# Kernel optimization log

Measured on AMD Instinct MI355X. Metric: run time of the kernel, lower is better.

## Reference

```python
import jax, jax.numpy as jnp
import numpy as np
from jax import lax

H, W, K, B = 64, 64, 64, 64
OFFSETS = [(0, 1), (2, 1), (1, 0), (1, 2)]  # up, down, left, right slices into padded grid


def setup_inputs() -> dict:
    key = jax.random.key(0)
    ks = jax.random.split(key, 7)
    n = H * W * 3
    s = lambda d: 1.0 / np.sqrt(d)
    return {
        "obs_flat": jax.random.normal(ks[0], (B, n), jnp.float32),
        "phi_w": jax.random.normal(ks[1], (n, n), jnp.float32) * s(n),
        "phi_b": jax.random.normal(ks[2], (n,), jnp.float32) * s(n),
        "w1": jax.random.normal(ks[3], (36, 16), jnp.float32) * s(36),
        "b1": jax.random.normal(ks[4], (16,), jnp.float32) * s(36),
        "w2": jax.random.normal(ks[5], (16, 4), jnp.float32) * s(16),
        "b2": jax.random.normal(ks[6], (4,), jnp.float32) * s(16),
    }


def _vin(rin, rout, p):
    # rin, rout, p: [B, H, W]. K Bellman-style 4-neighbor sweeps.
    prin = jnp.pad(rin, ((0, 0), (1, 1), (1, 1)))
    rin_sh = jnp.stack([prin[:, ho:ho + H, wo:wo + W] for ho, wo in OFFSETS])  # [4,B,H,W]
    rout_masked = rout[None] * (rin_sh != 0).astype(rin.dtype)                 # [4,B,H,W]

    def step(V, _):
        pv = jnp.pad(V, ((0, 0), (1, 1), (1, 1)))
        v_sh = jnp.stack([pv[:, ho:ho + H, wo:wo + W] for ho, wo in OFFSETS])
        nv = p[None] * v_sh + rin_sh - rout_masked
        return jnp.maximum(V, nv.max(axis=0)), None

    V0 = jnp.zeros_like(rin)
    V, _ = lax.scan(step, V0, None, length=K)
    return V


def reference(obs_flat, phi_w, phi_b, w1, b1, w2, b2):
    obs = obs_flat.reshape(B, H, W, 3)
    phi = (obs_flat @ phi_w + phi_b).reshape(B, H, W, 3)
    rin, rout = phi[..., 0], phi[..., 1]
    p = jax.nn.softmax(phi[..., 2].reshape(B, H * W), axis=1).reshape(B, H, W)

    V = _vin(rin, rout, p)  # [B,H,W]
    obs_val = jnp.concatenate([obs, V[..., None]], axis=-1)  # [B,H,W,4]
    padded = jnp.pad(obs_val, ((0, 0), (1, 1), (1, 1), (0, 0)))

    # agent position = location of the (one-hot) nonzero in channel 1
    flat = jnp.argmax(obs[..., 1].reshape(B, -1), axis=1)
    pi, pj = flat // W, flat % W
    patch = jax.vmap(lambda x, i, j: lax.dynamic_slice(x, (i, j, 0), (3, 3, 4)))(padded, pi, pj)

    h = jax.nn.relu(patch.reshape(B, 36) @ w1 + b1)
    logit = h @ w2 + b2  # [B, 4]
    return logit
```

## Files before the change

kernel.cpp:

```cpp
#include <hip/hip_runtime.h>
#include <hip/hip_bf16.h>

typedef __attribute__((ext_vector_type(8))) short short8;
typedef __attribute__((ext_vector_type(4))) float floatx4;
typedef __attribute__((ext_vector_type(4))) unsigned short ushort4v;
typedef __attribute__((ext_vector_type(8))) unsigned short ushort8v;

#define N_DIM 12288
#define SPLITK 4
#define KCHUNK (N_DIM / SPLITK)
#define KSTEP 64
#define NTILE 64

__device__ __forceinline__ unsigned short f2bf(float f) {
  union { float f; unsigned int i; } x; x.f = f;
  unsigned int r = x.i + 0x7fffu + ((x.i >> 16) & 1u);
  return (unsigned short)(r >> 16);
}

__global__ __launch_bounds__(256) void gemm_phi(
    const float* __restrict__ obs, const float* __restrict__ W,
    const float* __restrict__ bias, float* __restrict__ phi)
{
  __shared__ unsigned short A_s[64 * 72];
  __shared__ unsigned short W_s[64 * 72];

  const int t = threadIdx.x;
  const int n0 = blockIdx.x * NTILE;
  const int s  = blockIdx.y;
  const int k0 = s * KCHUNK;
  const int lane = t & 63, wv = t >> 6;
  const int l16 = lane & 15, q = lane >> 4;
  const int m0f = 16 * wv;

  floatx4 acc[4];
#pragma unroll
  for (int i = 0; i < 4; i++) acc[i] = (floatx4){0.f, 0.f, 0.f, 0.f};

  const int am = t >> 2, akq = (t & 3) * 16;
  const int rg = t >> 4, cg = t & 15;

  for (int it = 0; it < KCHUNK / KSTEP; ++it) {
    const int kb = k0 + it * KSTEP;
    {
      const float* src = obs + (size_t)am * N_DIM + kb + akq;
      floatx4 f0 = *(const floatx4*)(src);
      floatx4 f1 = *(const floatx4*)(src + 4);
      floatx4 f2 = *(const floatx4*)(src + 8);
      floatx4 f3 = *(const floatx4*)(src + 12);
      ushort8v u0, u1;
#pragma unroll
      for (int i = 0; i < 4; i++) {
        u0[i] = f2bf(f0[i]); u0[4 + i] = f2bf(f1[i]);
        u1[i] = f2bf(f2[i]); u1[4 + i] = f2bf(f3[i]);
      }
      *(ushort8v*)&A_s[am * 72 + akq]     = u0;
      *(ushort8v*)&A_s[am * 72 + akq + 8] = u1;
    }
    {
      const size_t base = (size_t)(kb + 4 * rg) * N_DIM + (n0 + 4 * cg);
      floatx4 r0 = *(const floatx4*)(W + base);
      floatx4 r1 = *(const floatx4*)(W + base + N_DIM);
      floatx4 r2 = *(const floatx4*)(W + base + 2 * N_DIM);
      floatx4 r3 = *(const floatx4*)(W + base + 3 * N_DIM);
#pragma unroll
      for (int i = 0; i < 4; i++) {
        ushort4v v = { f2bf(r0[i]), f2bf(r1[i]), f2bf(r2[i]), f2bf(r3[i]) };
        *(ushort4v*)&W_s[(4 * cg + i) * 72 + 4 * rg] = v;
      }
    }
    __syncthreads();
#pragma unroll
    for (int kk = 0; kk < 2; ++kk) {
      short8 af = *(const short8*)&A_s[(m0f + l16) * 72 + 32 * kk + 8 * q];
#pragma unroll
      for (int nt = 0; nt < 4; ++nt) {
        short8 wf = *(const short8*)&W_s[(16 * nt + l16) * 72 + 32 * kk + 8 * q];
        acc[nt] = __builtin_amdgcn_mfma_f32_16x16x32_bf16(af, wf, acc[nt], 0, 0, 0);
      }
    }
    __syncthreads();
  }
#pragma unroll
  for (int nt = 0; nt < 4; ++nt) {
    const int ncol = n0 + 16 * nt + l16;
    const float bv = (s == 0) ? bias[ncol] : 0.f;
#pragma unroll
    for (int r = 0; r < 4; ++r) {
      const int m = m0f + q * 4 + r;
      atomicAdd(&phi[(size_t)m * N_DIM + ncol], acc[nt][r] + bv);
    }
  }
}

#define VSTR 76
#define VOFF(h, w) (((h) + 1) * VSTR + (w) + 4)

__global__ __launch_bounds__(256) void vin_mlp(
    const float* __restrict__ obs, const float* __restrict__ phi,
    const float* __restrict__ w1, const float* __restrict__ b1,
    const float* __restrict__ w2, const float* __restrict__ b2,
    float* __restrict__ out)
{
  __shared__ float Vb[2][66 * VSTR];
  __shared__ float red_v[256];
  __shared__ int   red_i[256];

  const int b = blockIdx.x;
  const int t = threadIdx.x;
  const int ty = t >> 4, tx = t & 15;
  const int h0 = ty * 4, w0 = tx * 4;

  for (int i = t; i < 2 * 66 * VSTR; i += 256) (&Vb[0][0])[i] = 0.f;

  float rin[16], rout[16], lg[16];
#pragma unroll
  for (int r = 0; r < 4; r++) {
    const int j = 3 * ((h0 + r) * 64 + w0);
    const floatx4* p4 = (const floatx4*)(phi + (size_t)b * N_DIM + j);
    floatx4 x0 = p4[0], x1 = p4[1], x2 = p4[2];
    float f[12];
#pragma unroll
    for (int c = 0; c < 4; c++) { f[c] = x0[c]; f[4 + c] = x1[c]; f[8 + c] = x2[c]; }
#pragma unroll
    for (int c = 0; c < 4; c++) {
      rin [r * 4 + c] = f[3 * c + 0];
      rout[r * 4 + c] = f[3 * c + 1];
      lg  [r * 4 + c] = f[3 * c + 2];
    }
  }

  float lmax = -3.4e38f;
#pragma unroll
  for (int i = 0; i < 16; i++) lmax = fmaxf(lmax, lg[i]);
  __syncthreads();
  red_v[t] = lmax; __syncthreads();
  for (int o = 128; o > 0; o >>= 1) { if (t < o) red_v[t] = fmaxf(red_v[t], red_v[t + o]); __syncthreads(); }
  const float M = red_v[0];
  __syncthreads();
  float p[16]; float esum = 0.f;
#pragma unroll
  for (int i = 0; i < 16; i++) { p[i] = __expf(lg[i] - M); esum += p[i]; }
  red_v[t] = esum; __syncthreads();
  for (int o = 128; o > 0; o >>= 1) { if (t < o) red_v[t] += red_v[t + o]; __syncthreads(); }
  const float inv = 1.f / red_v[0];
  __syncthreads();
#pragma unroll
  for (int i = 0; i < 16; i++) p[i] *= inv;

#pragma unroll
  for (int r = 0; r < 4; r++) {
    floatx4 rr = { rin[r * 4 + 0], rin[r * 4 + 1], rin[r * 4 + 2], rin[r * 4 + 3] };
    *(floatx4*)&Vb[1][VOFF(h0 + r, w0)] = rr;
  }
  __syncthreads();
  float cu[16], cdn[16], cl[16], cr[16];
#pragma unroll
  for (int r = 0; r < 4; r++) {
#pragma unroll
    for (int c = 0; c < 4; c++) {
      const int i = r * 4 + c, h = h0 + r, w = w0 + c;
      const float nu = Vb[1][VOFF(h - 1, w)];
      const float nd = Vb[1][VOFF(h + 1, w)];
      const float nl = Vb[1][VOFF(h, w - 1)];
      const float nr = Vb[1][VOFF(h, w + 1)];
      cu [i] = nu - (nu != 0.f ? rout[i] : 0.f);
      cdn[i] = nd - (nd != 0.f ? rout[i] : 0.f);
      cl [i] = nl - (nl != 0.f ? rout[i] : 0.f);
      cr [i] = nr - (nr != 0.f ? rout[i] : 0.f);
    }
  }
  __syncthreads();

  float v[16];
#pragma unroll
  for (int i = 0; i < 16; i++) v[i] = 0.f;

  for (int k = 0; k < 64; k++) {
    const float* Vc = Vb[k & 1];
    float* Vn = Vb[(k & 1) ^ 1];
    const floatx4 top = *(const floatx4*)&Vc[VOFF(h0 - 1, w0)];
    const floatx4 bot = *(const floatx4*)&Vc[VOFF(h0 + 4, w0)];
    float lf[4], rt[4];
#pragma unroll
    for (int r = 0; r < 4; r++) { lf[r] = Vc[VOFF(h0 + r, w0 - 1)]; rt[r] = Vc[VOFF(h0 + r, w0 + 4)]; }
    float nv[16];
#pragma unroll
    for (int r = 0; r < 4; r++) {
#pragma unroll
      for (int c = 0; c < 4; c++) {
        const int i = r * 4 + c;
        const float vu = (r == 0) ? top[c] : v[i - 4];
        const float vd = (r == 3) ? bot[c] : v[i + 4];
        const float vl = (c == 0) ? lf[r] : v[i - 1];
        const float vr = (c == 3) ? rt[r] : v[i + 1];
        const float m1 = fmaxf(fmaf(p[i], vu, cu[i]), fmaf(p[i], vd, cdn[i]));
        const float m2 = fmaxf(fmaf(p[i], vl, cl[i]), fmaf(p[i], vr, cr[i]));
        nv[i] = fmaxf(v[i], fmaxf(m1, m2));
      }
    }
#pragma unroll
    for (int r = 0; r < 4; r++) {
      floatx4 w4 = { nv[r * 4 + 0], nv[r * 4 + 1], nv[r * 4 + 2], nv[r * 4 + 3] };
      *(floatx4*)&Vn[VOFF(h0 + r, w0)] = w4;
    }
#pragma unroll
    for (int i = 0; i < 16; i++) v[i] = nv[i];
    __syncthreads();
  }

  float amax = -3.4e38f; int aidx = 0;
#pragma unroll
  for (int r = 0; r < 4; r++) {
#pragma unroll
    for (int c = 0; c < 4; c++) {
      const int cell = (h0 + r) * 64 + (w0 + c);
      const float val = obs[(size_t)b * N_DIM + 3 * cell + 1];
      if (val > amax) { amax = val; aidx = cell; }
    }
  }
  red_v[t] = amax; red_i[t] = aidx;
  __syncthreads();
  for (int o = 128; o > 0; o >>= 1) {
    if (t < o) {
      const float v2 = red_v[t + o]; const int i2 = red_i[t + o];
      if (v2 > red_v[t] || (v2 == red_v[t] && i2 < red_i[t])) { red_v[t] = v2; red_i[t] = i2; }
    }
    __syncthreads();
  }
  const int pos = red_i[0];
  const int pi = pos >> 6, pj = pos & 63;
  __syncthreads();

  if (t < 36) {
    const int di = t / 12, rem = t % 12, dj = rem / 4, c4 = rem & 3;
    const int hh = pi - 1 + di, ww = pj - 1 + dj;
    float pv;
    if (c4 < 3) {
      pv = (hh >= 0 && hh < 64 && ww >= 0 && ww < 64)
           ? obs[(size_t)b * N_DIM + 3 * (hh * 64 + ww) + c4] : 0.f;
    } else {
      pv = Vb[0][VOFF(hh, ww)];
    }
    red_v[t] = pv;
  }
  __syncthreads();
  if (t < 16) {
    float a = b1[t];
#pragma unroll
    for (int j = 0; j < 36; j++) a = fmaf(red_v[j], w1[j * 16 + t], a);
    red_v[64 + t] = fmaxf(a, 0.f);
  }
  __syncthreads();
  if (t < 4) {
    float a = b2[t];
#pragma unroll
    for (int i = 0; i < 16; i++) a = fmaf(red_v[64 + i], w2[i * 4 + t], a);
    out[b * 4 + t] = a;
  }
}

extern "C" void kernel_launch(void* const* d_in, const int* in_sizes, int n_in,
                              void* d_out, int out_size, void* d_ws, size_t ws_size,
                              hipStream_t stream)
{
  (void)in_sizes; (void)n_in; (void)out_size; (void)ws_size;
  const float* obs  = (const float*)d_in[0];
  const float* phiw = (const float*)d_in[1];
  const float* phib = (const float*)d_in[2];
  const float* w1   = (const float*)d_in[3];
  const float* b1   = (const float*)d_in[4];
  const float* w2   = (const float*)d_in[5];
  const float* b2   = (const float*)d_in[6];
  float* phi = (float*)d_ws;
  float* out = (float*)d_out;

  hipMemsetAsync(phi, 0, (size_t)64 * N_DIM * sizeof(float), stream);
  hipLaunchKernelGGL(gemm_phi, dim3(N_DIM / NTILE, SPLITK), dim3(256), 0, stream,
                     obs, phiw, phib, phi);
  hipLaunchKernelGGL(vin_mlp, dim3(64), dim3(256), 0, stream,
                     obs, phi, w1, b1, w2, b2, out);
}
```

Before: 836.8 us.

## Double-buffer A tile, load W fragments directly to registers, raise split-K

Restructures the phi GEMM so each wave owns 16 output columns and loads its W fragment straight from global memory into registers, dropping the shared-memory transpose of W. The A tile is double-buffered in LDS and the next iteration's A and W loads are issued before the current MFMAs, leaving one barrier per step. Split-K rises from 4 to 8 to put more blocks on the device, in exchange for twice as many atomic adds into phi. The W loads are scalar strided reads, 16 lanes wide per row, which may hurt coalescing.

Result: no change. 841.9 us (+0.6%).

```diff
diff --git a/kernel.cpp b/kernel.cpp
--- a/kernel.cpp
+++ b/kernel.cpp
@@ -3,14 +3,12 @@
 
 typedef __attribute__((ext_vector_type(8))) short short8;
 typedef __attribute__((ext_vector_type(4))) float floatx4;
-typedef __attribute__((ext_vector_type(4))) unsigned short ushort4v;
 typedef __attribute__((ext_vector_type(8))) unsigned short ushort8v;
 
 #define N_DIM 12288
-#define SPLITK 4
+#define SPLITK 8
 #define KCHUNK (N_DIM / SPLITK)
-#define KSTEP 64
-#define NTILE 64
+#define NIT (KCHUNK / 64)
 
 __device__ __forceinline__ unsigned short f2bf(float f) {
   union { float f; unsigned int i; } x; x.f = f;
@@ -22,73 +20,100 @@
     const float* __restrict__ obs, const float* __restrict__ W,
     const float* __restrict__ bias, float* __restrict__ phi)
 {
-  __shared__ unsigned short A_s[64 * 72];
-  __shared__ unsigned short W_s[64 * 72];
+  __shared__ unsigned short A_s[2][64 * 72];
 
   const int t = threadIdx.x;
-  const int n0 = blockIdx.x * NTILE;
+  const int n0 = blockIdx.x * 64;
   const int s  = blockIdx.y;
   const int k0 = s * KCHUNK;
   const int lane = t & 63, wv = t >> 6;
   const int l16 = lane & 15, q = lane >> 4;
-  const int m0f = 16 * wv;
+  const int nc = n0 + 16 * wv + l16;
 
   floatx4 acc[4];
 #pragma unroll
   for (int i = 0; i < 4; i++) acc[i] = (floatx4){0.f, 0.f, 0.f, 0.f};
 
-  const int am = t >> 2, akq = (t & 3) * 16;
-  const int rg = t >> 4, cg = t & 15;
-
-  for (int it = 0; it < KCHUNK / KSTEP; ++it) {
-    const int kb = k0 + it * KSTEP;
-    {
-      const float* src = obs + (size_t)am * N_DIM + kb + akq;
-      floatx4 f0 = *(const floatx4*)(src);
-      floatx4 f1 = *(const floatx4*)(src + 4);
-      floatx4 f2 = *(const floatx4*)(src + 8);
-      floatx4 f3 = *(const floatx4*)(src + 12);
+  const int am = t >> 2, ak = (t & 3) * 16;
+  const float* Ap = obs + (size_t)am * N_DIM + k0 + ak;
+  const float* Bp = W + (size_t)(k0 + 8 * q) * N_DIM + nc;
+
+  float fb[16];
+  {
+    floatx4 fA[4];
+#pragma unroll
+    for (int i = 0; i < 4; i++) fA[i] = *(const floatx4*)(Ap + 4 * i);
+    ushort8v u0, u1;
+#pragma unroll
+    for (int i = 0; i < 4; i++) {
+      u0[i] = f2bf(fA[0][i]); u0[4 + i] = f2bf(fA[1][i]);
+      u1[i] = f2bf(fA[2][i]); u1[4 + i] = f2bf(fA[3][i]);
+    }
+    *(ushort8v*)&A_s[0][am * 72 + ak]     = u0;
+    *(ushort8v*)&A_s[0][am * 72 + ak + 8] = u1;
+#pragma unroll
+    for (int kk = 0; kk < 2; ++kk)
+#pragma unroll
+      for (int j = 0; j < 8; ++j)
+        fb[kk * 8 + j] = Bp[(size_t)(32 * kk + j) * N_DIM];
+  }
+  __syncthreads();
+
+#pragma unroll 2
+  for (int it = 0; it < NIT; ++it) {
+    const int cur = it & 1;
+    const bool more = (it + 1 < NIT);
+    floatx4 fA[4];
+    float fbn[16];
+    if (more) {
+      const float* ap = Ap + (it + 1) * 64;
+#pragma unroll
+      for (int i = 0; i < 4; i++) fA[i] = *(const floatx4*)(ap + 4 * i);
+      const float* bp = Bp + (size_t)(it + 1) * 64 * N_DIM;
+#pragma unroll
+      for (int kk = 0; kk < 2; ++kk)
+#pragma unroll
+        for (int j = 0; j < 8; ++j)
+          fbn[kk * 8 + j] = bp[(size_t)(32 * kk + j) * N_DIM];
+    }
+    short8 bfr0, bfr1;
+#pragma unroll
+    for (int j = 0; j < 8; ++j) {
+      bfr0[j] = (short)f2bf(fb[j]);
+      bfr1[j] = (short)f2bf(fb[8 + j]);
+    }
+#pragma unroll
+    for (int mt = 0; mt < 4; ++mt) {
+      short8 af0 = *(const short8*)&A_s[cur][(16 * mt + l16) * 72 + 8 * q];
+      acc[mt] = __builtin_amdgcn_mfma_f32_16x16x32_bf16(af0, bfr0, acc[mt], 0, 0, 0);
+    }
+#pragma unroll
+    for (int mt = 0; mt < 4; ++mt) {
+      short8 af1 = *(const short8*)&A_s[cur][(16 * mt + l16) * 72 + 32 + 8 * q];
+      acc[mt] = __builtin_amdgcn_mfma_f32_16x16x32_bf16(af1, bfr1, acc[mt], 0, 0, 0);
+    }
+    if (more) {
       ushort8v u0, u1;
 #pragma unroll
       for (int i = 0; i < 4; i++) {
-        u0[i] = f2bf(f0[i]); u0[4 + i] = f2bf(f1[i]);
-        u1[i] = f2bf(f2[i]); u1[4 + i] = f2bf(f3[i]);
+        u0[i] = f2bf(fA[0][i]); u0[4 + i] = f2bf(fA[1][i]);
+        u1[i] = f2bf(fA[2][i]); u1[4 + i] = f2bf(fA[3][i]);
       }
-      *(ushort8v*)&A_s[am * 72 + akq]     = u0;
-      *(ushort8v*)&A_s[am * 72 + akq + 8] = u1;
-    }
-    {
-      const size_t base = (size_t)(kb + 4 * rg) * N_DIM + (n0 + 4 * cg);
-      floatx4 r0 = *(const floatx4*)(W + base);
-      floatx4 r1 = *(const floatx4*)(W + base + N_DIM);
-      floatx4 r2 = *(const floatx4*)(W + base + 2 * N_DIM);
-      floatx4 r3 = *(const floatx4*)(W + base + 3 * N_DIM);
-#pragma unroll
-      for (int i = 0; i < 4; i++) {
-        ushort4v v = { f2bf(r0[i]), f2bf(r1[i]), f2bf(r2[i]), f2bf(r3[i]) };
-        *(ushort4v*)&W_s[(4 * cg + i) * 72 + 4 * rg] = v;
-      }
+      *(ushort8v*)&A_s[cur ^ 1][am * 72 + ak]     = u0;
+      *(ushort8v*)&A_s[cur ^ 1][am * 72 + ak + 8] = u1;
+#pragma unroll
+      for (int i = 0; i < 16; i++) fb[i] = fbn[i];
     }
     __syncthreads();
-#pragma unroll
-    for (int kk = 0; kk < 2; ++kk) {
-      short8 af = *(const short8*)&A_s[(m0f + l16) * 72 + 32 * kk + 8 * q];
-#pragma unroll
-      for (int nt = 0; nt < 4; ++nt) {
-        short8 wf = *(const short8*)&W_s[(16 * nt + l16) * 72 + 32 * kk + 8 * q];
-        acc[nt] = __builtin_amdgcn_mfma_f32_16x16x32_bf16(af, wf, acc[nt], 0, 0, 0);
-      }
-    }
-    __syncthreads();
-  }
-#pragma unroll
-  for (int nt = 0; nt < 4; ++nt) {
-    const int ncol = n0 + 16 * nt + l16;
-    const float bv = (s == 0) ? bias[ncol] : 0.f;
+  }
+
+  const float bv = (s == 0) ? bias[nc] : 0.f;
+#pragma unroll
+  for (int mt = 0; mt < 4; ++mt) {
 #pragma unroll
     for (int r = 0; r < 4; ++r) {
-      const int m = m0f + q * 4 + r;
-      atomicAdd(&phi[(size_t)m * N_DIM + ncol], acc[nt][r] + bv);
+      const int m = 16 * mt + 4 * q + r;
+      atomicAdd(&phi[(size_t)m * N_DIM + nc], acc[mt][r] + bv);
     }
   }
 }
@@ -276,7 +301,7 @@
   float* out = (float*)d_out;
 
   hipMemsetAsync(phi, 0, (size_t)64 * N_DIM * sizeof(float), stream);
-  hipLaunchKernelGGL(gemm_phi, dim3(N_DIM / NTILE, SPLITK), dim3(256), 0, stream,
+  hipLaunchKernelGGL(gemm_phi, dim3(N_DIM / 64, SPLITK), dim3(256), 0, stream,
                      obs, phiw, phib, phi);
   hipLaunchKernelGGL(vin_mlp, dim3(64), dim3(256), 0, stream,
                      obs, phi, w1, b1, w2, b2, out);
```
